# Kernel tuning notes

Hardware: AMD Instinct MI355X
Metric: run time of the kernel (lower is better)

The kernel has to match this reference:

```python
import jax, jax.numpy as jnp
import numpy as np

B = 8192
DIM = 64
NUM_USERS = 100000
NUM_ITEMS = 100000
GAMMA = 1.0


def setup_inputs() -> dict:
    key = jax.random.key(0)
    k1, k2, k3, k4, k5 = jax.random.split(key, 5)
    return {
        "user_id": jax.random.randint(k1, (B,), 0, NUM_USERS, dtype=jnp.int64)
        if jax.config.jax_enable_x64 else jax.random.randint(k1, (B,), 0, NUM_USERS, dtype=jnp.int32),
        "pos_id": jax.random.randint(k2, (B,), 0, NUM_ITEMS, dtype=jnp.int32),
        "neg_id": jax.random.randint(k3, (B,), 0, NUM_ITEMS, dtype=jnp.int32),
        "user_table": jax.random.normal(k4, (NUM_USERS, DIM), dtype=jnp.float32) * 0.01,
        "item_table": jax.random.normal(k5, (NUM_ITEMS, DIM), dtype=jnp.float32) * 0.01,
    }


def _normalize(x):
    return x / jnp.linalg.norm(x, axis=-1, keepdims=True)


def _alignment(x, y):
    # F.normalize then mean squared L2 distance over the batch
    xn, yn = _normalize(x), _normalize(y)
    return jnp.mean(jnp.sum((xn - yn) ** 2, axis=1))


def _uniformity(x):
    # log mean_{i<j} exp(-2 * ||xi - xj||^2) on normalized rows.
    # For unit vectors: ||xi - xj||^2 = 2 - 2 <xi, xj>. Use the full Gram
    # matrix; diagonal contributes exp(0)=1 per row, removed in closed form.
    xn = _normalize(x)
    n = xn.shape[0]
    sim = xn @ xn.T                      # [B, B]
    e = jnp.exp(-2.0 * (2.0 - 2.0 * sim))  # [B, B]
    pair_sum = (jnp.sum(e) - n) * 0.5    # sum over i<j
    n_pairs = n * (n - 1) // 2
    return jnp.log(pair_sum / n_pairs)


def reference(user_id, pos_id, neg_id, user_table, item_table):
    user_e = user_table[user_id]   # [B, DIM]
    pos_e = item_table[pos_id]     # [B, DIM]
    align = _alignment(user_e, pos_e)
    uniform = (_uniformity(user_e) + _uniformity(pos_e)) * 0.5
    return align + GAMMA * uniform
```

## Files before the change

kernel.cpp:

```cpp
#include <hip/hip_runtime.h>
#include <hip/hip_bf16.h>
#include <math.h>

#define NROWS 8192
#define DIM 64
#define NTILE 64
#define NPAIRS 2080

typedef __bf16 bf16x8 __attribute__((ext_vector_type(8)));
typedef float f32x4 __attribute__((ext_vector_type(4)));


__global__ __launch_bounds__(256) void gather_norm_kernel(
    const int* __restrict__ user_id, const int* __restrict__ pos_id,
    const float* __restrict__ user_table, const float* __restrict__ item_table,
    float* __restrict__ part_align,
    __hip_bfloat16* __restrict__ Xu, __hip_bfloat16* __restrict__ Xp)
{
    const int lane = threadIdx.x & 63;
    const int w    = threadIdx.x >> 6;
    const int row  = blockIdx.x * 4 + w;

    const float u = user_table[(long)user_id[row] * DIM + lane];
    const float p = item_table[(long)pos_id[row] * DIM + lane];

    float su = u * u, sp = p * p;
    #pragma unroll
    for (int m = 32; m >= 1; m >>= 1) {
        su += __shfl_xor(su, m, 64);
        sp += __shfl_xor(sp, m, 64);
    }
    const float un = u * rsqrtf(su);
    const float pn = p * rsqrtf(sp);

    Xu[row * DIM + lane] = __float2bfloat16(un);
    Xp[row * DIM + lane] = __float2bfloat16(pn);

    const float d = un - pn;
    float dd = d * d;
    #pragma unroll
    for (int m = 32; m >= 1; m >>= 1) dd += __shfl_xor(dd, m, 64);

    __shared__ float red[4];
    if (lane == 0) red[w] = dd;
    __syncthreads();
    if (threadIdx.x == 0)
        part_align[blockIdx.x] = red[0] + red[1] + red[2] + red[3];
}

__global__ __launch_bounds__(256) void gram_exp_kernel(
    const __hip_bfloat16* __restrict__ Xu, const __hip_bfloat16* __restrict__ Xp,
    float* __restrict__ part_gram)
{
    const int t = blockIdx.x;
    const int z = blockIdx.y;
    const __hip_bfloat16* __restrict__ X = (z == 0) ? Xu : Xp;

    int i = (int)((sqrtf(8.0f * (float)t + 1.0f) - 1.0f) * 0.5f);
    while (i * (i + 1) / 2 > t) --i;
    while ((i + 1) * (i + 2) / 2 <= t) ++i;
    const int j = t - i * (i + 1) / 2;
    const int bi = j, bj = i;

    const int tid  = threadIdx.x;
    const int lane = tid & 63;
    const int w    = tid >> 6;
    const int wr   = w >> 1, wc = w & 1;
    const int r    = lane & 15;
    const int koff = (lane >> 4) * 8;

    const int i_base = bi * 128 + wr * 64;
    const int j_base = bj * 128 + wc * 64;

    bf16x8 a[4][2], b[4][2];
    #pragma unroll
    for (int tt = 0; tt < 4; ++tt) {
        const __hip_bfloat16* pa = X + (i_base + tt * 16 + r) * DIM + koff;
        a[tt][0] = *reinterpret_cast<const bf16x8*>(pa);
        a[tt][1] = *reinterpret_cast<const bf16x8*>(pa + 32);
        const __hip_bfloat16* pb = X + (j_base + tt * 16 + r) * DIM + koff;
        b[tt][0] = *reinterpret_cast<const bf16x8*>(pb);
        b[tt][1] = *reinterpret_cast<const bf16x8*>(pb + 32);
    }

    f32x4 acc[4][4];
    #pragma unroll
    for (int mt = 0; mt < 4; ++mt)
        #pragma unroll
        for (int nt = 0; nt < 4; ++nt) {
            f32x4 c = {0.f, 0.f, 0.f, 0.f};
            c = __builtin_amdgcn_mfma_f32_16x16x32_bf16(a[mt][0], b[nt][0], c, 0, 0, 0);
            c = __builtin_amdgcn_mfma_f32_16x16x32_bf16(a[mt][1], b[nt][1], c, 0, 0, 0);
            acc[mt][nt] = c;
        }

    const float C4 = 5.770780163555851f;
    float s0 = 0.f, s1 = 0.f, s2 = 0.f, s3 = 0.f;
    #pragma unroll
    for (int mt = 0; mt < 4; ++mt)
        #pragma unroll
        for (int nt = 0; nt < 4; ++nt) {
            s0 += __builtin_amdgcn_exp2f(fmaf(C4, acc[mt][nt][0], -C4));
            s1 += __builtin_amdgcn_exp2f(fmaf(C4, acc[mt][nt][1], -C4));
            s2 += __builtin_amdgcn_exp2f(fmaf(C4, acc[mt][nt][2], -C4));
            s3 += __builtin_amdgcn_exp2f(fmaf(C4, acc[mt][nt][3], -C4));
        }
    float s = (s0 + s1) + (s2 + s3);

    #pragma unroll
    for (int m = 32; m >= 1; m >>= 1) s += __shfl_xor(s, m, 64);

    __shared__ float red[4];
    if (lane == 0) red[w] = s;
    __syncthreads();
    if (tid == 0) {
        const float wgt = (bi == bj) ? 1.f : 2.f;
        part_gram[z * NPAIRS + t] = wgt * (red[0] + red[1] + red[2] + red[3]);
    }
}

__global__ __launch_bounds__(256) void finalize_kernel(
    const float* __restrict__ part_align, const float* __restrict__ part_gram,
    float* __restrict__ out)
{
    float a = 0.f, su = 0.f, sp = 0.f;
    for (int k = threadIdx.x; k < 2048; k += 256)   a  += part_align[k];
    for (int k = threadIdx.x; k < NPAIRS; k += 256) su += part_gram[k];
    for (int k = threadIdx.x; k < NPAIRS; k += 256) sp += part_gram[NPAIRS + k];

    #pragma unroll
    for (int m = 32; m >= 1; m >>= 1) {
        a  += __shfl_xor(a, m, 64);
        su += __shfl_xor(su, m, 64);
        sp += __shfl_xor(sp, m, 64);
    }
    __shared__ float ra[4], ru[4], rp[4];
    const int w = threadIdx.x >> 6, lane = threadIdx.x & 63;
    if (lane == 0) { ra[w] = a; ru[w] = su; rp[w] = sp; }
    __syncthreads();
    if (threadIdx.x == 0) {
        const float A  = ra[0] + ra[1] + ra[2] + ra[3];
        const float SU = ru[0] + ru[1] + ru[2] + ru[3];
        const float SP = rp[0] + rp[1] + rp[2] + rp[3];
        const float n = 8192.f;
        const float npairs = 8192.f * 8191.f * 0.5f;
        const float pu = (SU - n) * 0.5f;
        const float pp = (SP - n) * 0.5f;
        out[0] = A / n + 0.5f * (logf(pu / npairs) + logf(pp / npairs));
    }
}

extern "C" void kernel_launch(void* const* d_in, const int* in_sizes, int n_in,
                              void* d_out, int out_size, void* d_ws, size_t ws_size,
                              hipStream_t stream)
{
    const int*   user_id    = (const int*)d_in[0];
    const int*   pos_id     = (const int*)d_in[1];
    const float* user_table = (const float*)d_in[3];
    const float* item_table = (const float*)d_in[4];
    float* out = (float*)d_out;

    float* part_align = (float*)d_ws;
    float* part_gram  = (float*)((char*)d_ws + 8192);
    __hip_bfloat16* Xu = (__hip_bfloat16*)((char*)d_ws + 32768);
    __hip_bfloat16* Xp = Xu + (size_t)NROWS * DIM;

    gather_norm_kernel<<<NROWS / 4, 256, 0, stream>>>(
        user_id, pos_id, user_table, item_table, part_align, Xu, Xp);

    gram_exp_kernel<<<dim3(NPAIRS, 2), 256, 0, stream>>>(Xu, Xp, part_gram);

    finalize_kernel<<<1, 256, 0, stream>>>(part_align, part_gram, out);
}
```

Baseline: 133.4 us.

## Fuse gather, gram-exp, and finalize into one cooperative persistent kernel

Replaces the three launches with a single cooperative persistent kernel that gathers and normalizes rows, runs the tiled gram-exp jobs in a grid-stride loop, and finalizes on block 0, with grid-wide syncs between phases. It also removes the per-block shared-memory reduction and syncthreads in the gram job, writing one partial per wave instead, so finalize reads four times as many partials. The aim is to cut launch gaps and intra-block barriers, at the cost of grid sync overhead and an occupancy query on the host every call. If the cooperative launch fails, it falls back to three separate kernels.

```diff
diff --git a/kernel.cpp b/kernel.cpp
--- a/kernel.cpp
+++ b/kernel.cpp
@@ -1,29 +1,29 @@
 #include <hip/hip_runtime.h>
 #include <hip/hip_bf16.h>
+#include <hip/hip_cooperative_groups.h>
 #include <math.h>
+
+namespace cg = cooperative_groups;
 
 #define NROWS 8192
 #define DIM 64
 #define NTILE 64
 #define NPAIRS 2080
+#define NJOBS (2 * NPAIRS)
 
 typedef __bf16 bf16x8 __attribute__((ext_vector_type(8)));
 typedef float f32x4 __attribute__((ext_vector_type(4)));
 
 
-__global__ __launch_bounds__(256) void gather_norm_kernel(
-    const int* __restrict__ user_id, const int* __restrict__ pos_id,
-    const float* __restrict__ user_table, const float* __restrict__ item_table,
-    float* __restrict__ part_align,
+
+__device__ __forceinline__ float gather_row(
+    int row, int lane,
+    const int* __restrict__ uid, const int* __restrict__ pid,
+    const float* __restrict__ ut, const float* __restrict__ it,
     __hip_bfloat16* __restrict__ Xu, __hip_bfloat16* __restrict__ Xp)
 {
-    const int lane = threadIdx.x & 63;
-    const int w    = threadIdx.x >> 6;
-    const int row  = blockIdx.x * 4 + w;
-
-    const float u = user_table[(long)user_id[row] * DIM + lane];
-    const float p = item_table[(long)pos_id[row] * DIM + lane];
-
+    const float u = ut[(long)uid[row] * DIM + lane];
+    const float p = it[(long)pid[row] * DIM + lane];
     float su = u * u, sp = p * p;
     #pragma unroll
     for (int m = 32; m >= 1; m >>= 1) {
@@ -32,29 +32,23 @@
     }
     const float un = u * rsqrtf(su);
     const float pn = p * rsqrtf(sp);
-
     Xu[row * DIM + lane] = __float2bfloat16(un);
     Xp[row * DIM + lane] = __float2bfloat16(pn);
-
     const float d = un - pn;
     float dd = d * d;
     #pragma unroll
     for (int m = 32; m >= 1; m >>= 1) dd += __shfl_xor(dd, m, 64);
-
-    __shared__ float red[4];
-    if (lane == 0) red[w] = dd;
-    __syncthreads();
-    if (threadIdx.x == 0)
-        part_align[blockIdx.x] = red[0] + red[1] + red[2] + red[3];
-}
-
-__global__ __launch_bounds__(256) void gram_exp_kernel(
+    return dd;
+}
+
+__device__ __forceinline__ void gram_job(
+    int t4, int tid,
     const __hip_bfloat16* __restrict__ Xu, const __hip_bfloat16* __restrict__ Xp,
     float* __restrict__ part_gram)
 {
-    const int t = blockIdx.x;
-    const int z = blockIdx.y;
-    const __hip_bfloat16* __restrict__ X = (z == 0) ? Xu : Xp;
+    const int z = (t4 >= NPAIRS) ? 1 : 0;
+    const int t = t4 - z * NPAIRS;
+    const __hip_bfloat16* __restrict__ X = z ? Xp : Xu;
 
     int i = (int)((sqrtf(8.0f * (float)t + 1.0f) - 1.0f) * 0.5f);
     while (i * (i + 1) / 2 > t) --i;
@@ -62,7 +56,6 @@
     const int j = t - i * (i + 1) / 2;
     const int bi = j, bj = i;
 
-    const int tid  = threadIdx.x;
     const int lane = tid & 63;
     const int w    = tid >> 6;
     const int wr   = w >> 1, wc = w & 1;
@@ -106,28 +99,21 @@
             s3 += __builtin_amdgcn_exp2f(fmaf(C4, acc[mt][nt][3], -C4));
         }
     float s = (s0 + s1) + (s2 + s3);
-
     #pragma unroll
     for (int m = 32; m >= 1; m >>= 1) s += __shfl_xor(s, m, 64);
 
-    __shared__ float red[4];
-    if (lane == 0) red[w] = s;
-    __syncthreads();
-    if (tid == 0) {
-        const float wgt = (bi == bj) ? 1.f : 2.f;
-        part_gram[z * NPAIRS + t] = wgt * (red[0] + red[1] + red[2] + red[3]);
-    }
-}
-
-__global__ __launch_bounds__(256) void finalize_kernel(
-    const float* __restrict__ part_align, const float* __restrict__ part_gram,
-    float* __restrict__ out)
+    if (lane == 0)
+        part_gram[t4 * 4 + w] = ((bi == bj) ? 1.f : 2.f) * s;
+}
+
+__device__ __forceinline__ void finalize_block(
+    const float* __restrict__ pa, const float* __restrict__ pg,
+    float* __restrict__ out, int tid, int na)
 {
     float a = 0.f, su = 0.f, sp = 0.f;
-    for (int k = threadIdx.x; k < 2048; k += 256)   a  += part_align[k];
-    for (int k = threadIdx.x; k < NPAIRS; k += 256) su += part_gram[k];
-    for (int k = threadIdx.x; k < NPAIRS; k += 256) sp += part_gram[NPAIRS + k];
-
+    for (int k = tid; k < na; k += 256)          a  += pa[k];
+    for (int k = tid; k < 4 * NPAIRS; k += 256)  su += pg[k];
+    for (int k = tid; k < 4 * NPAIRS; k += 256)  sp += pg[4 * NPAIRS + k];
     #pragma unroll
     for (int m = 32; m >= 1; m >>= 1) {
         a  += __shfl_xor(a, m, 64);
@@ -135,40 +121,113 @@
         sp += __shfl_xor(sp, m, 64);
     }
     __shared__ float ra[4], ru[4], rp[4];
-    const int w = threadIdx.x >> 6, lane = threadIdx.x & 63;
+    const int w = tid >> 6, lane = tid & 63;
     if (lane == 0) { ra[w] = a; ru[w] = su; rp[w] = sp; }
     __syncthreads();
-    if (threadIdx.x == 0) {
+    if (tid == 0) {
         const float A  = ra[0] + ra[1] + ra[2] + ra[3];
         const float SU = ru[0] + ru[1] + ru[2] + ru[3];
         const float SP = rp[0] + rp[1] + rp[2] + rp[3];
         const float n = 8192.f;
         const float npairs = 8192.f * 8191.f * 0.5f;
-        const float pu = (SU - n) * 0.5f;
-        const float pp = (SP - n) * 0.5f;
-        out[0] = A / n + 0.5f * (logf(pu / npairs) + logf(pp / npairs));
-    }
-}
+        out[0] = A / n + 0.5f * (logf((SU - n) * 0.5f / npairs)
+                               + logf((SP - n) * 0.5f / npairs));
+    }
+}
+
+
+__global__ __launch_bounds__(256) void fused_kernel(
+    const int* __restrict__ uid, const int* __restrict__ pid,
+    const float* __restrict__ ut, const float* __restrict__ it,
+    float* __restrict__ part_align, float* __restrict__ part_gram,
+    __hip_bfloat16* __restrict__ Xu, __hip_bfloat16* __restrict__ Xp,
+    float* __restrict__ out)
+{
+    const int tid  = threadIdx.x;
+    const int lane = tid & 63;
+    const int w    = tid >> 6;
+    const int wave_gid  = blockIdx.x * 4 + w;
+    const int num_waves = gridDim.x * 4;
+
+    float dd = 0.f;
+    for (int row = wave_gid; row < NROWS; row += num_waves)
+        dd += gather_row(row, lane, uid, pid, ut, it, Xu, Xp);
+    if (lane == 0) part_align[wave_gid] = dd;
+
+    __threadfence();
+    cg::this_grid().sync();
+
+    for (int t4 = blockIdx.x; t4 < NJOBS; t4 += gridDim.x)
+        gram_job(t4, tid, Xu, Xp, part_gram);
+
+    __threadfence();
+    cg::this_grid().sync();
+
+    if (blockIdx.x == 0)
+        finalize_block(part_align, part_gram, out, tid, num_waves);
+}
+
+
+__global__ __launch_bounds__(256) void k_gather(
+    const int* __restrict__ uid, const int* __restrict__ pid,
+    const float* __restrict__ ut, const float* __restrict__ it,
+    float* __restrict__ part_align,
+    __hip_bfloat16* __restrict__ Xu, __hip_bfloat16* __restrict__ Xp)
+{
+    const int lane = threadIdx.x & 63, w = threadIdx.x >> 6;
+    const int row = blockIdx.x * 4 + w;
+    const float dd = gather_row(row, lane, uid, pid, ut, it, Xu, Xp);
+    if (lane == 0) part_align[row] = dd;
+}
+
+__global__ __launch_bounds__(256) void k_gram(
+    const __hip_bfloat16* __restrict__ Xu, const __hip_bfloat16* __restrict__ Xp,
+    float* __restrict__ part_gram)
+{
+    gram_job(blockIdx.x, threadIdx.x, Xu, Xp, part_gram);
+}
+
+__global__ __launch_bounds__(256) void k_final(
+    const float* __restrict__ pa, const float* __restrict__ pg,
+    float* __restrict__ out)
+{
+    finalize_block(pa, pg, out, threadIdx.x, NROWS);
+}
+
 
 extern "C" void kernel_launch(void* const* d_in, const int* in_sizes, int n_in,
                               void* d_out, int out_size, void* d_ws, size_t ws_size,
                               hipStream_t stream)
 {
-    const int*   user_id    = (const int*)d_in[0];
-    const int*   pos_id     = (const int*)d_in[1];
-    const float* user_table = (const float*)d_in[3];
-    const float* item_table = (const float*)d_in[4];
+    const int*   uid = (const int*)d_in[0];
+    const int*   pid = (const int*)d_in[1];
+    const float* ut  = (const float*)d_in[3];
+    const float* it  = (const float*)d_in[4];
     float* out = (float*)d_out;
 
     float* part_align = (float*)d_ws;
-    float* part_gram  = (float*)((char*)d_ws + 8192);
-    __hip_bfloat16* Xu = (__hip_bfloat16*)((char*)d_ws + 32768);
+    float* part_gram  = (float*)((char*)d_ws + 32768);
+    __hip_bfloat16* Xu = (__hip_bfloat16*)((char*)d_ws + 131072);
     __hip_bfloat16* Xp = Xu + (size_t)NROWS * DIM;
 
-    gather_norm_kernel<<<NROWS / 4, 256, 0, stream>>>(
-        user_id, pos_id, user_table, item_table, part_align, Xu, Xp);
-
-    gram_exp_kernel<<<dim3(NPAIRS, 2), 256, 0, stream>>>(Xu, Xp, part_gram);
-
-    finalize_kernel<<<1, 256, 0, stream>>>(part_align, part_gram, out);
-}
+    int nb = 0;
+    hipError_t qe = hipOccupancyMaxActiveBlocksPerMultiprocessor(
+        &nb, (const void*)fused_kernel, 256, 0);
+    int grid = (qe == hipSuccess && nb > 0) ? nb * 256 : 0;
+    if (grid > 2048) grid = 2048;
+
+    hipError_t err = hipErrorUnknown;
+    if (grid > 0) {
+        void* args[] = {(void*)&uid, (void*)&pid, (void*)&ut, (void*)&it,
+                        (void*)&part_align, (void*)&part_gram,
+                        (void*)&Xu, (void*)&Xp, (void*)&out};
+        err = hipLaunchCooperativeKernel((const void*)fused_kernel,
+                                         dim3(grid), dim3(256), args, 0, stream);
+    }
+    if (err != hipSuccess) {
+        (void)hipGetLastError();
+        k_gather<<<NROWS / 4, 256, 0, stream>>>(uid, pid, ut, it, part_align, Xu, Xp);
+        k_gram<<<NJOBS, 256, 0, stream>>>(Xu, Xp, part_gram);
+        k_final<<<1, 256, 0, stream>>>(part_align, part_gram, out);
+    }
+}
```

Result: slower. 309.0 us (+131.6%).
